# Optimization experiments

Hardware: AMD Instinct MI355X
Metric: run time of the kernel (lower is better)

Reference implementation:

```python
import jax, jax.numpy as jnp
import numpy as np

N_NODES = 50000
N_EDGES = 1600000
N_GRAPHS = 128
IN_C, HID, N_CLS = 128, 256, 10


def setup_inputs() -> dict:
    key = jax.random.key(0)
    ks = jax.random.split(key, 8)
    x = jax.random.normal(ks[0], (N_NODES, IN_C), dtype=jnp.float32)
    edge_index = jax.random.randint(ks[1], (2, N_EDGES), 0, N_NODES, dtype=jnp.int64)
    batch = jnp.sort(jax.random.randint(ks[2], (N_NODES,), 0, N_GRAPHS, dtype=jnp.int64))
    def glorot(k, shape):
        lim = np.sqrt(6.0 / (shape[0] + shape[1]))
        return jax.random.uniform(k, shape, jnp.float32, -lim, lim)
    return {
        "x": x, "edge_index": edge_index, "batch": batch,
        "W1": glorot(ks[3], (IN_C, HID)), "b1": jnp.zeros((HID,), jnp.float32),
        "W2": glorot(ks[4], (HID, HID)), "b2": jnp.zeros((HID,), jnp.float32),
        "Wl1": glorot(ks[5], (HID, 64)), "bl1": jnp.zeros((64,), jnp.float32),
        "Wl2": glorot(ks[6], (64, N_CLS)), "bl2": jnp.zeros((N_CLS,), jnp.float32),
    }


def _gcn_conv(x, row, col, deg_inv_sqrt, W, b):
    h = x @ W                                  # [N, out]
    norm = deg_inv_sqrt[row] * deg_inv_sqrt[col]   # [E]
    msg = h[row] * norm[:, None]                   # gather + scale
    agg = jax.ops.segment_sum(msg, col, num_segments=x.shape[0])
    agg = agg + h * (deg_inv_sqrt * deg_inv_sqrt)[:, None]  # self-loop term (norm = 1/deg)
    return agg + b


def reference(x, edge_index, batch, W1, b1, W2, b2, Wl1, bl1, Wl2, bl2):
    N = x.shape[0]
    row, col = edge_index[0], edge_index[1]
    # degree including self-loop, computed on target nodes (PyG convention)
    deg = jax.ops.segment_sum(jnp.ones((row.shape[0],), x.dtype), col, num_segments=N) + 1.0
    deg_inv_sqrt = jax.lax.rsqrt(deg)

    h = jax.nn.relu(_gcn_conv(x, row, col, deg_inv_sqrt, W1, b1))
    h = jax.nn.relu(_gcn_conv(h, row, col, deg_inv_sqrt, W2, b2))

    # global_mean_pool over batch ids
    sums = jax.ops.segment_sum(h, batch, num_segments=N_GRAPHS)
    cnts = jax.ops.segment_sum(jnp.ones((N,), h.dtype), batch, num_segments=N_GRAPHS)
    g = sums / jnp.maximum(cnts, 1.0)[:, None]     # [G, HID]

    g = jax.nn.relu(g @ Wl1 + bl1)
    return jax.nn.log_softmax(g @ Wl2 + bl2, axis=1)
```

## Files before the change

### kernel.cpp

```cpp
#include <hip/hip_runtime.h>
#include <hip/hip_bf16.h>
#include <math.h>

#define NN 50000
#define NG 128
#define INC 128
#define HIDC 256
#define NCLS 10

#define NBLK 256
#define BSH 8
#define NB 196

typedef __attribute__((ext_vector_type(8))) short s8_t;
typedef __attribute__((ext_vector_type(4))) float f4_t;

__device__ inline f4_t mfma16(s8_t a, s8_t b, f4_t c) {
  return __builtin_amdgcn_mfma_f32_16x16x32_bf16(a, b, c, 0, 0, 0);
}

__device__ inline float bf2f(ushort u) {
  union { unsigned int i; float f; } c; c.i = ((unsigned int)u) << 16; return c.f;
}
__device__ inline ushort f2bf(float f) {
  __hip_bfloat16 h = __float2bfloat16(f);
  return *(ushort*)&h;
}

__device__ inline void gload_lds16(const void* g, void* l) {
  __builtin_amdgcn_global_load_lds(
      (const __attribute__((address_space(1))) unsigned int*)g,
      (__attribute__((address_space(3))) unsigned int*)l, 16, 0, 0);
}

__global__ __launch_bounds__(256) void edge_hist(const int* __restrict__ ecol,
                                                 int* __restrict__ hist, int E, int chunk) {
  __shared__ int h[NB];
  int blk = blockIdx.x;
  for (int i = threadIdx.x; i < NB; i += 256) h[i] = 0;
  __syncthreads();
  int e0 = blk * chunk, e1 = min(e0 + chunk, E);
  for (int e = e0 + threadIdx.x; e < e1; e += 256)
    atomicAdd(&h[ecol[e] >> BSH], 1);
  __syncthreads();
  for (int i = threadIdx.x; i < NB; i += 256) hist[i * NBLK + blk] = h[i];
}

__global__ __launch_bounds__(256) void edge_partition(const int* __restrict__ erow,
                                                      const int* __restrict__ ecol,
                                                      const int* __restrict__ histBase,
                                                      uint2* __restrict__ part,
                                                      int E, int chunk) {
  __shared__ int cur[NB];
  int blk = blockIdx.x;
  for (int i = threadIdx.x; i < NB; i += 256) cur[i] = histBase[i * NBLK + blk];
  __syncthreads();
  int e0 = blk * chunk, e1 = min(e0 + chunk, E);
  for (int e = e0 + threadIdx.x; e < e1; e += 256) {
    int c = ecol[e];
    int b = c >> BSH;
    int pos = atomicAdd(&cur[b], 1);
    part[pos] = make_uint2((unsigned)erow[e], (unsigned)c);
  }
}

__global__ __launch_bounds__(256) void bucket_deg(const uint2* __restrict__ part,
                                                  const int* __restrict__ histBase,
                                                  int* __restrict__ deg, int N) {
  __shared__ int cnt[256];
  int b = blockIdx.x;
  cnt[threadIdx.x] = 0;
  __syncthreads();
  int s0 = histBase[b * NBLK];
  int s1 = histBase[(b + 1) * NBLK];
  for (int e = s0 + threadIdx.x; e < s1; e += 256)
    atomicAdd(&cnt[part[e].y & 255], 1);
  __syncthreads();
  int node = (b << BSH) + threadIdx.x;
  if (node < N) deg[node] = cnt[threadIdx.x];
}

__global__ __launch_bounds__(256) void bucket_csr(const uint2* __restrict__ part,
                                                  const int* __restrict__ histBase,
                                                  const int* __restrict__ offsets,
                                                  int* __restrict__ rows_csr, int N) {
  __shared__ int cur[256];
  int b = blockIdx.x;
  int node = (b << BSH) + threadIdx.x;
  cur[threadIdx.x] = (node < N) ? offsets[node] : 0;
  __syncthreads();
  int s0 = histBase[b * NBLK];
  int s1 = histBase[(b + 1) * NBLK];
  for (int e = s0 + threadIdx.x; e < s1; e += 256) {
    uint2 p = part[e];
    int pos = atomicAdd(&cur[p.y & 255], 1);
    rows_csr[pos] = (int)p.x;
  }
}

__global__ void compute_dis(const int* __restrict__ deg, float* __restrict__ dis, int n) {
  int i = blockIdx.x * blockDim.x + threadIdx.x;
  if (i < n) dis[i] = rsqrtf((float)deg[i] + 1.0f);
}

#define SCAN_T 256
#define SCAN_V 8
#define SCAN_VPB (SCAN_T * SCAN_V)

__global__ __launch_bounds__(SCAN_T) void scanA(const int* __restrict__ deg,
                                                int* __restrict__ offsets,
                                                int* __restrict__ blockTotals, int n) {
  __shared__ int sm[SCAN_T];
  int b = blockIdx.x;
  int t = threadIdx.x;
  int base = b * SCAN_VPB + t * SCAN_V;
  int v[SCAN_V];
  int run = 0;
  #pragma unroll
  for (int j = 0; j < SCAN_V; ++j) {
    int idx = base + j;
    int d = (idx < n) ? deg[idx] : 0;
    run += d;
    v[j] = run;
  }
  sm[t] = run;
  __syncthreads();
  #pragma unroll
  for (int off = 1; off < SCAN_T; off <<= 1) {
    int x = (t >= off) ? sm[t - off] : 0;
    __syncthreads();
    sm[t] += x;
    __syncthreads();
  }
  int excl = (t == 0) ? 0 : sm[t - 1];
  #pragma unroll
  for (int j = 0; j < SCAN_V; ++j) {
    int idx = base + j;
    if (idx < n) offsets[idx + 1] = v[j] + excl;
  }
  if (t == SCAN_T - 1) blockTotals[b] = sm[t];
}

__global__ void scanB(int* __restrict__ blockTotals, int nb) {
  if (threadIdx.x == 0 && blockIdx.x == 0) {
    int run = 0;
    for (int i = 0; i < nb; ++i) {
      int v = blockTotals[i];
      blockTotals[i] = run;
      run += v;
    }
  }
}

__global__ void scanC(int* __restrict__ offsets, const int* __restrict__ blockTotals, int n) {
  int stride = gridDim.x * blockDim.x;
  for (int i = blockIdx.x * blockDim.x + threadIdx.x; i < n; i += stride) {
    offsets[i + 1] += blockTotals[i / SCAN_VPB];
    if (i == 0) offsets[0] = 0;
  }
}

__global__ void cast_f32_bf16(const float* __restrict__ in, ushort* __restrict__ out, int n4) {
  int i = blockIdx.x * blockDim.x + threadIdx.x;
  if (i < n4) {
    float4 v = ((const float4*)in)[i];
    ushort4 o;
    o.x = f2bf(v.x); o.y = f2bf(v.y); o.z = f2bf(v.z); o.w = f2bf(v.w);
    ((ushort4*)out)[i] = o;
  }
}

__global__ void transpose_cast(const float* __restrict__ W, ushort* __restrict__ WT,
                               int K, int N) {
  int idx = blockIdx.x * blockDim.x + threadIdx.x;
  if (idx < K * N) {
    int k = idx / N, n = idx % N;
    WT[(long)n * K + k] = f2bf(W[idx]);
  }
}

__global__ __launch_bounds__(256) void aggregate128_bf16(
    const ushort* __restrict__ xb, const float* __restrict__ dis,
    const int* __restrict__ offsets, const int* __restrict__ rows_csr,
    ushort* __restrict__ outb, int N) {
  int node = blockIdx.x * 4 + (threadIdx.x >> 6);
  if (node >= N) return;
  int lane = threadIdx.x & 63;
  float di = dis[node];
  const unsigned int* xv = (const unsigned int*)xb;
  unsigned int sv = xv[(long)node * 64 + lane];
  float a0 = bf2f((ushort)sv) * di * di;
  float a1 = bf2f((ushort)(sv >> 16)) * di * di;
  int e0 = offsets[node], e1 = offsets[node + 1];
  int e = e0;
  for (; e + 3 < e1; e += 4) {
    int r0 = rows_csr[e], r1 = rows_csr[e + 1];
    int r2 = rows_csr[e + 2], r3 = rows_csr[e + 3];
    float s0 = dis[r0] * di, s1 = dis[r1] * di;
    float s2 = dis[r2] * di, s3 = dis[r3] * di;
    unsigned int v0 = xv[(long)r0 * 64 + lane];
    unsigned int v1 = xv[(long)r1 * 64 + lane];
    unsigned int v2 = xv[(long)r2 * 64 + lane];
    unsigned int v3 = xv[(long)r3 * 64 + lane];
    a0 = fmaf(bf2f((ushort)v0), s0, a0); a1 = fmaf(bf2f((ushort)(v0 >> 16)), s0, a1);
    a0 = fmaf(bf2f((ushort)v1), s1, a0); a1 = fmaf(bf2f((ushort)(v1 >> 16)), s1, a1);
    a0 = fmaf(bf2f((ushort)v2), s2, a0); a1 = fmaf(bf2f((ushort)(v2 >> 16)), s2, a1);
    a0 = fmaf(bf2f((ushort)v3), s3, a0); a1 = fmaf(bf2f((ushort)(v3 >> 16)), s3, a1);
  }
  for (; e < e1; ++e) {
    int r0 = rows_csr[e];
    float s0 = dis[r0] * di;
    unsigned int v0 = xv[(long)r0 * 64 + lane];
    a0 = fmaf(bf2f((ushort)v0), s0, a0); a1 = fmaf(bf2f((ushort)(v0 >> 16)), s0, a1);
  }
  unsigned int o = (unsigned int)f2bf(a0) | ((unsigned int)f2bf(a1) << 16);
  ((unsigned int*)outb)[(long)node * 64 + lane] = o;
}

__global__ __launch_bounds__(256) void aggregate256_bf16(
    const ushort* __restrict__ xb, const float* __restrict__ dis,
    const int* __restrict__ offsets, const int* __restrict__ rows_csr,
    ushort* __restrict__ outb, int N) {
  int node = blockIdx.x * 4 + (threadIdx.x >> 6);
  if (node >= N) return;
  int lane = threadIdx.x & 63;
  float di = dis[node];
  const uint2* xv = (const uint2*)xb;
  uint2 sv = xv[(long)node * 64 + lane];
  float a0 = bf2f((ushort)sv.x) * di * di;
  float a1 = bf2f((ushort)(sv.x >> 16)) * di * di;
  float a2 = bf2f((ushort)sv.y) * di * di;
  float a3 = bf2f((ushort)(sv.y >> 16)) * di * di;
  int e0 = offsets[node], e1 = offsets[node + 1];
  int e = e0;
  for (; e + 3 < e1; e += 4) {
    int r0 = rows_csr[e], r1 = rows_csr[e + 1];
    int r2 = rows_csr[e + 2], r3 = rows_csr[e + 3];
    float s0 = dis[r0] * di, s1 = dis[r1] * di;
    float s2 = dis[r2] * di, s3 = dis[r3] * di;
    uint2 v0 = xv[(long)r0 * 64 + lane];
    uint2 v1 = xv[(long)r1 * 64 + lane];
    uint2 v2 = xv[(long)r2 * 64 + lane];
    uint2 v3 = xv[(long)r3 * 64 + lane];
    a0 = fmaf(bf2f((ushort)v0.x), s0, a0); a1 = fmaf(bf2f((ushort)(v0.x >> 16)), s0, a1);
    a2 = fmaf(bf2f((ushort)v0.y), s0, a2); a3 = fmaf(bf2f((ushort)(v0.y >> 16)), s0, a3);
    a0 = fmaf(bf2f((ushort)v1.x), s1, a0); a1 = fmaf(bf2f((ushort)(v1.x >> 16)), s1, a1);
    a2 = fmaf(bf2f((ushort)v1.y), s1, a2); a3 = fmaf(bf2f((ushort)(v1.y >> 16)), s1, a3);
    a0 = fmaf(bf2f((ushort)v2.x), s2, a0); a1 = fmaf(bf2f((ushort)(v2.x >> 16)), s2, a1);
    a2 = fmaf(bf2f((ushort)v2.y), s2, a2); a3 = fmaf(bf2f((ushort)(v2.y >> 16)), s2, a3);
    a0 = fmaf(bf2f((ushort)v3.x), s3, a0); a1 = fmaf(bf2f((ushort)(v3.x >> 16)), s3, a1);
    a2 = fmaf(bf2f((ushort)v3.y), s3, a2); a3 = fmaf(bf2f((ushort)(v3.y >> 16)), s3, a3);
  }
  for (; e < e1; ++e) {
    int r0 = rows_csr[e];
    float s0 = dis[r0] * di;
    uint2 v0 = xv[(long)r0 * 64 + lane];
    a0 = fmaf(bf2f((ushort)v0.x), s0, a0); a1 = fmaf(bf2f((ushort)(v0.x >> 16)), s0, a1);
    a2 = fmaf(bf2f((ushort)v0.y), s0, a2); a3 = fmaf(bf2f((ushort)(v0.y >> 16)), s0, a3);
  }
  uint2 o;
  o.x = (unsigned int)f2bf(a0) | ((unsigned int)f2bf(a1) << 16);
  o.y = (unsigned int)f2bf(a2) | ((unsigned int)f2bf(a3) << 16);
  ((uint2*)outb)[(long)node * 64 + lane] = o;
}

template <int K, bool OUTBF16>
__global__ __launch_bounds__(256) void gemm_mfma(
    const ushort* __restrict__ A, const ushort* __restrict__ WT,
    const float* __restrict__ bias, ushort* __restrict__ outb,
    float* __restrict__ outf, int M) {
  __shared__ ushort smem[16384];
  const int tid = threadIdx.x;
  const int lane = tid & 63;
  const int wave = tid >> 6;
  const int wm = wave >> 1, wn = wave & 1;
  const int m0 = blockIdx.x * 128;
  const int n0 = blockIdx.y * 128;

  f4_t acc[4][4] = {};

  for (int k0 = 0; k0 < K; k0 += 64) {
    __syncthreads();
    #pragma unroll
    for (int is = 0; is < 4; ++is) {
      int s = is * 256 + tid;
      int row = s >> 3;
      int ch = (s & 7) ^ (row & 7);
      long grow = m0 + row; if (grow > M - 1) grow = M - 1;
      const ushort* g = A + grow * K + k0 + ch * 8;
      gload_lds16(g, &smem[(is * 256 + wave * 64) * 8]);
    }
    #pragma unroll
    for (int is = 0; is < 4; ++is) {
      int s = is * 256 + tid;
      int row = s >> 3;
      int ch = (s & 7) ^ (row & 7);
      const ushort* g = WT + (long)(n0 + row) * K + k0 + ch * 8;
      gload_lds16(g, &smem[8192 + (is * 256 + wave * 64) * 8]);
    }
    asm volatile("s_waitcnt vmcnt(0)" ::: "memory");
    __syncthreads();
    #pragma unroll
    for (int ks = 0; ks < 2; ++ks) {
      s8_t af[4], bfr[4];
      #pragma unroll
      for (int mi = 0; mi < 4; ++mi) {
        int row = wm * 64 + mi * 16 + (lane & 15);
        int ch = (ks * 4 + (lane >> 4)) ^ (row & 7);
        af[mi] = *(const s8_t*)(&smem[row * 64 + ch * 8]);
      }
      #pragma unroll
      for (int ni = 0; ni < 4; ++ni) {
        int row = wn * 64 + ni * 16 + (lane & 15);
        int ch = (ks * 4 + (lane >> 4)) ^ (row & 7);
        bfr[ni] = *(const s8_t*)(&smem[8192 + row * 64 + ch * 8]);
      }
      #pragma unroll
      for (int mi = 0; mi < 4; ++mi)
        #pragma unroll
        for (int ni = 0; ni < 4; ++ni)
          acc[mi][ni] = mfma16(af[mi], bfr[ni], acc[mi][ni]);
    }
  }
  #pragma unroll
  for (int ni = 0; ni < 4; ++ni) {
    int col = n0 + wn * 64 + ni * 16 + (lane & 15);
    float bb = bias[col];
    #pragma unroll
    for (int mi = 0; mi < 4; ++mi) {
      #pragma unroll
      for (int r = 0; r < 4; ++r) {
        int row = m0 + wm * 64 + mi * 16 + (lane >> 4) * 4 + r;
        if (row < M) {
          float v = fmaxf(acc[mi][ni][r] + bb, 0.0f);
          if (OUTBF16) outb[(long)row * HIDC + col] = f2bf(v);
          else outf[(long)row * HIDC + col] = v;
        }
      }
    }
  }
}

__global__ void find_bounds(const int* __restrict__ batch, int* __restrict__ gstart, int n) {
  int stride = gridDim.x * blockDim.x;
  for (int i = blockIdx.x * blockDim.x + threadIdx.x; i < n; i += stride) {
    int b = batch[i];
    if (i == 0) {
      for (int g = 0; g <= b; ++g) gstart[g] = 0;
    } else {
      int pb = batch[i - 1];
      if (pb != b)
        for (int g = pb + 1; g <= b; ++g) gstart[g] = i;
    }
    if (i == n - 1) {
      for (int g = b + 1; g <= NG; ++g) gstart[g] = n;
    }
  }
}

#define POOL_SPLIT 8
__global__ __launch_bounds__(HIDC) void pool_range_bf16(const ushort* __restrict__ h,
                                                        const int* __restrict__ gstart,
                                                        float* __restrict__ gsum) {
  int g = blockIdx.x;
  int s = blockIdx.y;
  int c = threadIdx.x;
  int s0 = gstart[g], s1 = gstart[g + 1];
  int len = s1 - s0;
  int chunk = (len + POOL_SPLIT - 1) / POOL_SPLIT;
  int i0 = s0 + s * chunk;
  int i1 = min(i0 + chunk, s1);
  float acc = 0.0f;
  for (int i = i0; i < i1; ++i) acc += bf2f(h[(long)i * HIDC + c]);
  if (i1 > i0) atomicAdd(&gsum[g * HIDC + c], acc);
}

__global__ __launch_bounds__(64) void mlp_kernel(
    const float* __restrict__ gsum, const int* __restrict__ gstart,
    const float* __restrict__ Wl1, const float* __restrict__ bl1,
    const float* __restrict__ Wl2, const float* __restrict__ bl2,
    float* __restrict__ out) {
  __shared__ float g[HIDC];
  __shared__ float hid[64];
  __shared__ float logits[NCLS];
  __shared__ float red[2];
  int i = blockIdx.x;
  int t = threadIdx.x;
  int cnt = gstart[i + 1] - gstart[i];
  float inv = 1.0f / fmaxf((float)cnt, 1.0f);
  for (int c = t; c < HIDC; c += 64) g[c] = gsum[i * HIDC + c] * inv;
  __syncthreads();
  float acc = bl1[t];
  for (int c = 0; c < HIDC; ++c) acc = fmaf(g[c], Wl1[c * 64 + t], acc);
  hid[t] = fmaxf(acc, 0.0f);
  __syncthreads();
  if (t < NCLS) {
    float l = bl2[t];
    for (int c = 0; c < 64; ++c) l = fmaf(hid[c], Wl2[c * NCLS + t], l);
    logits[t] = l;
  }
  __syncthreads();
  if (t == 0) {
    float m = -1e30f;
    for (int k = 0; k < NCLS; ++k) m = fmaxf(m, logits[k]);
    float s = 0.f;
    for (int k = 0; k < NCLS; ++k) s += expf(logits[k] - m);
    red[0] = m;
    red[1] = logf(s);
  }
  __syncthreads();
  if (t < NCLS) out[i * NCLS + t] = logits[t] - red[0] - red[1];
}

extern "C" void kernel_launch(void* const* d_in, const int* in_sizes, int n_in,
                              void* d_out, int out_size, void* d_ws, size_t ws_size,
                              hipStream_t stream) {
  const float* x = (const float*)d_in[0];
  const int* edge_index = (const int*)d_in[1];
  const int* batch = (const int*)d_in[2];
  const float* W1 = (const float*)d_in[3];
  const float* b1 = (const float*)d_in[4];
  const float* W2 = (const float*)d_in[5];
  const float* b2 = (const float*)d_in[6];
  const float* Wl1 = (const float*)d_in[7];
  const float* bl1 = (const float*)d_in[8];
  const float* Wl2 = (const float*)d_in[9];
  const float* bl2 = (const float*)d_in[10];
  float* out = (float*)d_out;

  const int N = in_sizes[0] / INC;
  const int E = in_sizes[1] / 2;
  const int* erow = edge_index;
  const int* ecol = edge_index + E;

  char* p = (char*)d_ws;
  auto alloc = [&](size_t bytes) {
    void* r = (void*)p;
    p += (bytes + 255) & ~(size_t)255;
    return r;
  };
  int* deg = (int*)alloc((size_t)N * 4);
  float* dis = (float*)alloc((size_t)N * 4);
  int* offsets = (int*)alloc((size_t)(N + 1) * 4);
  int* rows_csr = (int*)alloc((size_t)E * 4);
  uint2* part = (uint2*)alloc((size_t)E * 8);
  int* hist = (int*)alloc((size_t)(NB * NBLK) * 4);
  int* histBase = (int*)alloc((size_t)(NB * NBLK + 1) * 4);
  float* gsum = (float*)alloc((size_t)NG * HIDC * 4);
  int* gstart = (int*)alloc((size_t)(NG + 1) * 4);
  int* blockTotals = (int*)alloc((size_t)256 * 4);
  ushort* W1T = (ushort*)alloc((size_t)INC * HIDC * 2);
  ushort* W2T = (ushort*)alloc((size_t)HIDC * HIDC * 2);
  ushort* xb = (ushort*)alloc((size_t)N * INC * 2);
  ushort* agg1b = (ushort*)alloc((size_t)N * INC * 2);
  ushort* h1b = (ushort*)alloc((size_t)N * HIDC * 2);
  ushort* agg2b = (ushort*)alloc((size_t)N * HIDC * 2);
  ushort* h2b = xb;

  hipMemsetAsync(gsum, 0, (size_t)NG * HIDC * 4, stream);

  const int chunk = (E + NBLK - 1) / NBLK;
  edge_hist<<<NBLK, 256, 0, stream>>>(ecol, hist, E, chunk);
  {
    const int nh = NB * NBLK;
    const int nbh = (nh + SCAN_VPB - 1) / SCAN_VPB;
    scanA<<<nbh, SCAN_T, 0, stream>>>(hist, histBase, blockTotals, nh);
    scanB<<<1, 64, 0, stream>>>(blockTotals, nbh);
    scanC<<<(nh + 255) / 256, 256, 0, stream>>>(histBase, blockTotals, nh);
  }
  edge_partition<<<NBLK, 256, 0, stream>>>(erow, ecol, histBase, part, E, chunk);
  bucket_deg<<<NB, 256, 0, stream>>>(part, histBase, deg, N);
  compute_dis<<<(N + 255) / 256, 256, 0, stream>>>(deg, dis, N);
  {
    const int nb = (N + SCAN_VPB - 1) / SCAN_VPB;
    scanA<<<nb, SCAN_T, 0, stream>>>(deg, offsets, blockTotals, N);
    scanB<<<1, 64, 0, stream>>>(blockTotals, nb);
    scanC<<<(N + 255) / 256, 256, 0, stream>>>(offsets, blockTotals, N);
  }
  bucket_csr<<<NB, 256, 0, stream>>>(part, histBase, offsets, rows_csr, N);

  cast_f32_bf16<<<(N * INC / 4 + 255) / 256, 256, 0, stream>>>(x, xb, N * INC / 4);
  transpose_cast<<<(INC * HIDC + 255) / 256, 256, 0, stream>>>(W1, W1T, INC, HIDC);
  transpose_cast<<<(HIDC * HIDC + 255) / 256, 256, 0, stream>>>(W2, W2T, HIDC, HIDC);

  aggregate128_bf16<<<(N + 3) / 4, 256, 0, stream>>>(xb, dis, offsets, rows_csr, agg1b, N);
  {
    dim3 grid((N + 127) / 128, HIDC / 128);
    gemm_mfma<INC, true><<<grid, 256, 0, stream>>>(agg1b, W1T, b1, h1b, nullptr, N);
  }
  aggregate256_bf16<<<(N + 3) / 4, 256, 0, stream>>>(h1b, dis, offsets, rows_csr, agg2b, N);
  {
    dim3 grid((N + 127) / 128, HIDC / 128);
    gemm_mfma<HIDC, true><<<grid, 256, 0, stream>>>(agg2b, W2T, b2, h2b, nullptr, N);
  }
  find_bounds<<<(N + 255) / 256, 256, 0, stream>>>(batch, gstart, N);
  {
    dim3 pgrid(NG, POOL_SPLIT);
    pool_range_bf16<<<pgrid, HIDC, 0, stream>>>(h2b, gstart, gsum);
  }
  mlp_kernel<<<NG, 64, 0, stream>>>(gsum, gstart, Wl1, bl1, Wl2, bl2, out);
}
```

Before: 419.9 us.

## Pack edge partition entries, fuse small kernels, and widen GEMM tile to full N

Edge partition entries are packed into one 32-bit word (row shifted left by 8, low 8 bits of col), halving partition traffic. compute_dis is folded into the bucket degree kernel, and the two weight transpose-casts are merged into one launch. The MFMA GEMM now computes all 256 output columns per block (128x256 tile, larger LDS and accumulators), so each A tile is loaded once instead of twice. The cost is higher register and LDS use per block and half as many blocks, which can lower occupancy. The packing only holds while node ids fit in 24 bits.

```diff
diff --git a/kernel.cpp b/kernel.cpp
--- a/kernel.cpp
+++ b/kernel.cpp
@@ -49,7 +49,7 @@
 __global__ __launch_bounds__(256) void edge_partition(const int* __restrict__ erow,
                                                       const int* __restrict__ ecol,
                                                       const int* __restrict__ histBase,
-                                                      uint2* __restrict__ part,
+                                                      unsigned* __restrict__ part,
                                                       int E, int chunk) {
   __shared__ int cur[NB];
   int blk = blockIdx.x;
@@ -60,13 +60,14 @@
     int c = ecol[e];
     int b = c >> BSH;
     int pos = atomicAdd(&cur[b], 1);
-    part[pos] = make_uint2((unsigned)erow[e], (unsigned)c);
-  }
-}
-
-__global__ __launch_bounds__(256) void bucket_deg(const uint2* __restrict__ part,
-                                                  const int* __restrict__ histBase,
-                                                  int* __restrict__ deg, int N) {
+    part[pos] = ((unsigned)erow[e] << 8) | (unsigned)(c & 255);
+  }
+}
+
+__global__ __launch_bounds__(256) void bucket_deg_dis(const unsigned* __restrict__ part,
+                                                      const int* __restrict__ histBase,
+                                                      int* __restrict__ deg,
+                                                      float* __restrict__ dis, int N) {
   __shared__ int cnt[256];
   int b = blockIdx.x;
   cnt[threadIdx.x] = 0;
@@ -74,13 +75,17 @@
   int s0 = histBase[b * NBLK];
   int s1 = histBase[(b + 1) * NBLK];
   for (int e = s0 + threadIdx.x; e < s1; e += 256)
-    atomicAdd(&cnt[part[e].y & 255], 1);
+    atomicAdd(&cnt[part[e] & 255], 1);
   __syncthreads();
   int node = (b << BSH) + threadIdx.x;
-  if (node < N) deg[node] = cnt[threadIdx.x];
-}
-
-__global__ __launch_bounds__(256) void bucket_csr(const uint2* __restrict__ part,
+  if (node < N) {
+    int d = cnt[threadIdx.x];
+    deg[node] = d;
+    dis[node] = rsqrtf((float)d + 1.0f);
+  }
+}
+
+__global__ __launch_bounds__(256) void bucket_csr(const unsigned* __restrict__ part,
                                                   const int* __restrict__ histBase,
                                                   const int* __restrict__ offsets,
                                                   int* __restrict__ rows_csr, int N) {
@@ -92,15 +97,10 @@
   int s0 = histBase[b * NBLK];
   int s1 = histBase[(b + 1) * NBLK];
   for (int e = s0 + threadIdx.x; e < s1; e += 256) {
-    uint2 p = part[e];
-    int pos = atomicAdd(&cur[p.y & 255], 1);
-    rows_csr[pos] = (int)p.x;
-  }
-}
-
-__global__ void compute_dis(const int* __restrict__ deg, float* __restrict__ dis, int n) {
-  int i = blockIdx.x * blockDim.x + threadIdx.x;
-  if (i < n) dis[i] = rsqrtf((float)deg[i] + 1.0f);
+    unsigned pv = part[e];
+    int pos = atomicAdd(&cur[pv & 255], 1);
+    rows_csr[pos] = (int)(pv >> 8);
+  }
 }
 
 #define SCAN_T 256
@@ -170,12 +170,17 @@
   }
 }
 
-__global__ void transpose_cast(const float* __restrict__ W, ushort* __restrict__ WT,
-                               int K, int N) {
+__global__ void transpose_cast2(const float* __restrict__ W1, ushort* __restrict__ W1T,
+                                const float* __restrict__ W2, ushort* __restrict__ W2T) {
   int idx = blockIdx.x * blockDim.x + threadIdx.x;
-  if (idx < K * N) {
-    int k = idx / N, n = idx % N;
-    WT[(long)n * K + k] = f2bf(W[idx]);
+  if (idx < INC * HIDC) {
+    int k = idx / HIDC, n = idx % HIDC;
+    W1T[(long)n * INC + k] = f2bf(W1[idx]);
+  }
+  int i2 = idx - INC * HIDC;
+  if (i2 >= 0 && i2 < HIDC * HIDC) {
+    int k = i2 / HIDC, n = i2 % HIDC;
+    W2T[(long)n * HIDC + k] = f2bf(W2[i2]);
   }
 }
 
@@ -264,20 +269,18 @@
   ((uint2*)outb)[(long)node * 64 + lane] = o;
 }
 
-template <int K, bool OUTBF16>
+template <int K>
 __global__ __launch_bounds__(256) void gemm_mfma(
     const ushort* __restrict__ A, const ushort* __restrict__ WT,
-    const float* __restrict__ bias, ushort* __restrict__ outb,
-    float* __restrict__ outf, int M) {
-  __shared__ ushort smem[16384];
+    const float* __restrict__ bias, ushort* __restrict__ outb, int M) {
+  __shared__ ushort smem[24576];
   const int tid = threadIdx.x;
   const int lane = tid & 63;
   const int wave = tid >> 6;
   const int wm = wave >> 1, wn = wave & 1;
   const int m0 = blockIdx.x * 128;
-  const int n0 = blockIdx.y * 128;
-
-  f4_t acc[4][4] = {};
+
+  f4_t acc[4][8] = {};
 
   for (int k0 = 0; k0 < K; k0 += 64) {
     __syncthreads();
@@ -287,22 +290,21 @@
       int row = s >> 3;
       int ch = (s & 7) ^ (row & 7);
       long grow = m0 + row; if (grow > M - 1) grow = M - 1;
-      const ushort* g = A + grow * K + k0 + ch * 8;
-      gload_lds16(g, &smem[(is * 256 + wave * 64) * 8]);
+      gload_lds16(A + grow * K + k0 + ch * 8, &smem[(is * 256 + wave * 64) * 8]);
     }
     #pragma unroll
-    for (int is = 0; is < 4; ++is) {
-      int s = is * 256 + tid;
+    for (int ib = 0; ib < 8; ++ib) {
+      int s = ib * 256 + tid;
       int row = s >> 3;
       int ch = (s & 7) ^ (row & 7);
-      const ushort* g = WT + (long)(n0 + row) * K + k0 + ch * 8;
-      gload_lds16(g, &smem[8192 + (is * 256 + wave * 64) * 8]);
+      gload_lds16(WT + (long)row * K + k0 + ch * 8,
+                  &smem[8192 + (ib * 256 + wave * 64) * 8]);
     }
     asm volatile("s_waitcnt vmcnt(0)" ::: "memory");
     __syncthreads();
     #pragma unroll
     for (int ks = 0; ks < 2; ++ks) {
-      s8_t af[4], bfr[4];
+      s8_t af[4];
       #pragma unroll
       for (int mi = 0; mi < 4; ++mi) {
         int row = wm * 64 + mi * 16 + (lane & 15);
@@ -310,21 +312,19 @@
         af[mi] = *(const s8_t*)(&smem[row * 64 + ch * 8]);
       }
       #pragma unroll
-      for (int ni = 0; ni < 4; ++ni) {
-        int row = wn * 64 + ni * 16 + (lane & 15);
-        int ch = (ks * 4 + (lane >> 4)) ^ (row & 7);
-        bfr[ni] = *(const s8_t*)(&smem[8192 + row * 64 + ch * 8]);
+      for (int ni = 0; ni < 8; ++ni) {
+        int brow = wn * 128 + ni * 16 + (lane & 15);
+        int ch = (ks * 4 + (lane >> 4)) ^ (brow & 7);
+        s8_t bf = *(const s8_t*)(&smem[8192 + brow * 64 + ch * 8]);
+        #pragma unroll
+        for (int mi = 0; mi < 4; ++mi)
+          acc[mi][ni] = mfma16(af[mi], bf, acc[mi][ni]);
       }
-      #pragma unroll
-      for (int mi = 0; mi < 4; ++mi)
-        #pragma unroll
-        for (int ni = 0; ni < 4; ++ni)
-          acc[mi][ni] = mfma16(af[mi], bfr[ni], acc[mi][ni]);
     }
   }
   #pragma unroll
-  for (int ni = 0; ni < 4; ++ni) {
-    int col = n0 + wn * 64 + ni * 16 + (lane & 15);
+  for (int ni = 0; ni < 8; ++ni) {
+    int col = wn * 128 + ni * 16 + (lane & 15);
     float bb = bias[col];
     #pragma unroll
     for (int mi = 0; mi < 4; ++mi) {
@@ -333,8 +333,7 @@
         int row = m0 + wm * 64 + mi * 16 + (lane >> 4) * 4 + r;
         if (row < M) {
           float v = fmaxf(acc[mi][ni][r] + bb, 0.0f);
-          if (OUTBF16) outb[(long)row * HIDC + col] = f2bf(v);
-          else outf[(long)row * HIDC + col] = v;
+          outb[(long)row * HIDC + col] = f2bf(v);
         }
       }
     }
@@ -443,7 +442,7 @@
   float* dis = (float*)alloc((size_t)N * 4);
   int* offsets = (int*)alloc((size_t)(N + 1) * 4);
   int* rows_csr = (int*)alloc((size_t)E * 4);
-  uint2* part = (uint2*)alloc((size_t)E * 8);
+  unsigned* part = (unsigned*)alloc((size_t)E * 4);
   int* hist = (int*)alloc((size_t)(NB * NBLK) * 4);
   int* histBase = (int*)alloc((size_t)(NB * NBLK + 1) * 4);
   float* gsum = (float*)alloc((size_t)NG * HIDC * 4);
@@ -469,8 +468,7 @@
     scanC<<<(nh + 255) / 256, 256, 0, stream>>>(histBase, blockTotals, nh);
   }
   edge_partition<<<NBLK, 256, 0, stream>>>(erow, ecol, histBase, part, E, chunk);
-  bucket_deg<<<NB, 256, 0, stream>>>(part, histBase, deg, N);
-  compute_dis<<<(N + 255) / 256, 256, 0, stream>>>(deg, dis, N);
+  bucket_deg_dis<<<NB, 256, 0, stream>>>(part, histBase, deg, dis, N);
   {
     const int nb = (N + SCAN_VPB - 1) / SCAN_VPB;
     scanA<<<nb, SCAN_T, 0, stream>>>(deg, offsets, blockTotals, N);
@@ -480,19 +478,15 @@
   bucket_csr<<<NB, 256, 0, stream>>>(part, histBase, offsets, rows_csr, N);
 
   cast_f32_bf16<<<(N * INC / 4 + 255) / 256, 256, 0, stream>>>(x, xb, N * INC / 4);
-  transpose_cast<<<(INC * HIDC + 255) / 256, 256, 0, stream>>>(W1, W1T, INC, HIDC);
-  transpose_cast<<<(HIDC * HIDC + 255) / 256, 256, 0, stream>>>(W2, W2T, HIDC, HIDC);
+  {
+    int tot = INC * HIDC + HIDC * HIDC;
+    transpose_cast2<<<(tot + 255) / 256, 256, 0, stream>>>(W1, W1T, W2, W2T);
+  }
 
   aggregate128_bf16<<<(N + 3) / 4, 256, 0, stream>>>(xb, dis, offsets, rows_csr, agg1b, N);
-  {
-    dim3 grid((N + 127) / 128, HIDC / 128);
-    gemm_mfma<INC, true><<<grid, 256, 0, stream>>>(agg1b, W1T, b1, h1b, nullptr, N);
-  }
+  gemm_mfma<INC><<<(N + 127) / 128, 256, 0, stream>>>(agg1b, W1T, b1, h1b, N);
   aggregate256_bf16<<<(N + 3) / 4, 256, 0, stream>>>(h1b, dis, offsets, rows_csr, agg2b, N);
-  {
-    dim3 grid((N + 127) / 128, HIDC / 128);
-    gemm_mfma<HIDC, true><<<grid, 256, 0, stream>>>(agg2b, W2T, b2, h2b, nullptr, N);
-  }
+  gemm_mfma<HIDC><<<(N + 127) / 128, 256, 0, stream>>>(agg2b, W2T, b2, h2b, N);
   find_bounds<<<(N + 255) / 256, 256, 0, stream>>>(batch, gstart, N);
   {
     dim3 pgrid(NG, POOL_SPLIT);
```

After: 435.0 us. 1.04x slower.
